# Kernel tuning notes

Measured on AMD Instinct MI355X. Metric: run time of the kernel, lower is better.

Reference implementation:

```python
import jax, jax.numpy as jnp
import numpy as np

B, N, C, H = 64, 300, 256, 8  # batch, patches (img 1x300, patch 1x1), dim, heads
STD = 0.02


def setup_inputs() -> dict:
    key = jax.random.key(0)
    ks = jax.random.split(key, 6)
    return {
        "x": jax.random.normal(ks[0], (B, N, C), jnp.float32),
        "Wqk": jax.random.normal(ks[1], (2 * C, C), jnp.float32) * STD,
        "Wv": jax.random.normal(ks[2], (C, C), jnp.float32) * STD,
        "Wpos": jax.random.normal(ks[3], (H, 3), jnp.float32) * STD,
        "bpos": jnp.zeros((H,), jnp.float32),
        "Wproj": jax.random.normal(ks[4], (C, C), jnp.float32) * STD,
        "bproj": jnp.zeros((C,), jnp.float32),
        "gating": jnp.ones((H,), jnp.float32),
    }


def _rel_indices(n):
    d = (jnp.arange(n)[None, :] - jnp.arange(n)[:, None]).astype(jnp.float32)
    return jnp.stack([d, jnp.zeros_like(d), d * d], axis=-1)  # [N, N, 3]


def reference(x, Wqk, Wv, Wpos, bpos, Wproj, bproj, gating):
    Bb, Nn, Cc = x.shape
    Hh = gating.shape[0]
    hd = Cc // Hh
    scale = hd ** -0.5

    qk = (x @ Wqk.T).reshape(Bb, Nn, 2, Hh, hd)
    q = qk[:, :, 0].transpose(0, 2, 1, 3)  # [B,H,N,hd]
    k = qk[:, :, 1].transpose(0, 2, 1, 3)

    patch_score = jax.nn.softmax(jnp.einsum('bhnd,bhmd->bhnm', q, k) * scale, axis=-1)

    rel = _rel_indices(Nn)                               # [N,N,3]
    pos_score = (rel @ Wpos.T + bpos).transpose(2, 0, 1)  # [H,N,N]
    pos_score = jax.nn.softmax(pos_score, axis=-1)

    g = jax.nn.sigmoid(gating)[None, :, None, None]       # [1,H,1,1]
    attn = (1.0 - g) * patch_score + g * pos_score[None]
    attn = attn / attn.sum(axis=-1, keepdims=True)

    v = (x @ Wv.T).reshape(Bb, Nn, Hh, hd).transpose(0, 2, 1, 3)  # [B,H,N,hd]
    out = jnp.einsum('bhnm,bhmd->bhnd', attn, v)
    out = out.transpose(0, 2, 1, 3).reshape(Bb, Nn, Cc)
    return out @ Wproj.T + bproj
```

## Files before the change

kernel.cpp:

```cpp
#include <hip/hip_runtime.h>


#define NSEQ 300
#define HEADS 8
#define HD 32

typedef short v8s __attribute__((ext_vector_type(8)));
typedef float v4f __attribute__((ext_vector_type(4)));
typedef unsigned int v4u __attribute__((ext_vector_type(4)));

__device__ __forceinline__ ushort f2bf(float f) {
    unsigned u = __float_as_uint(f);
    u = (u + 0x7FFFu + ((u >> 16) & 1u)) >> 16;
    return (ushort)u;
}

__device__ __forceinline__ unsigned pk2bf(float a, float b) {
    unsigned ua = __float_as_uint(a), ub = __float_as_uint(b);
    ua += 0x7FFFu + ((ua >> 16) & 1u);
    ub += 0x7FFFu + ((ub >> 16) & 1u);
    return __builtin_amdgcn_perm(ub, ua, 0x07060302);
}

__device__ __forceinline__ unsigned cvtpk(float a, float b) {
    unsigned r;
    asm("v_cvt_pk_bf16_f32 %0, %1, %2" : "=v"(r) : "v"(a), "v"(b));
    return r;
}

__device__ __forceinline__ float fexp2(float x) {
    float r; asm("v_exp_f32 %0, %1" : "=v"(r) : "v"(x)); return r;
}

__device__ __forceinline__ void gl_lds16(const ushort* g, ushort* l) {
    __builtin_amdgcn_global_load_lds(
        (const __attribute__((address_space(1))) void*)g,
        (__attribute__((address_space(3))) void*)l, 16, 0, 0);
}

__global__ __launch_bounds__(256) void prep_kernel(
    const float* __restrict__ Wqk, const float* __restrict__ Wv,
    const float* __restrict__ Wproj, const float* __restrict__ Wpos,
    const float* __restrict__ bpos, const float* __restrict__ gating,
    ushort* __restrict__ Wf, ushort* __restrict__ wproj_t,
    ushort* __restrict__ gpos)
{
    int bid = blockIdx.x, tid = threadIdx.x;
    if (bid < 608) {
        int sub = bid;
        int h = sub / 76;
        int i = (sub % 76) * 4 + (tid >> 6);
        int lane = tid & 63;
        ushort* gr = gpos + ((size_t)h * 304 + i) * 304;
        if (i >= NSEQ) {
#pragma unroll
            for (int t = 0; t < 5; ++t) {
                int j = lane + 64 * t;
                if (j < 304) gr[j] = 0;
            }
            return;
        }
        float w0 = Wpos[h * 3 + 0], w2 = Wpos[h * 3 + 2], bb = bpos[h];
        float g = 1.f / (1.f + __expf(-gating[h]));
        float sv[5]; float m2 = -1e30f;
#pragma unroll
        for (int t = 0; t < 5; ++t) {
            int j = lane + 64 * t;
            float d = (float)(j - i);
            float lg = fmaf(w2, d * d, fmaf(w0, d, bb));
            sv[t] = (j < NSEQ) ? lg : -1e30f;
            m2 = fmaxf(m2, sv[t]);
        }
#pragma unroll
        for (int off = 32; off > 0; off >>= 1) m2 = fmaxf(m2, __shfl_xor(m2, off));
        float sum = 0.f;
#pragma unroll
        for (int t = 0; t < 5; ++t) { sv[t] = __expf(sv[t] - m2); sum += sv[t]; }
#pragma unroll
        for (int off = 32; off > 0; off >>= 1) sum += __shfl_xor(sum, off);
        float gi = g / sum;
#pragma unroll
        for (int t = 0; t < 5; ++t) {
            int j = lane + 64 * t;
            if (j < NSEQ) gr[j] = f2bf(sv[t] * gi);
            else if (j < 304) gr[j] = 0;
        }
        return;
    }
    if (bid < 704) {
        int idx = (bid - 608) * 256 + tid;
        int c = idx & 7;
        int t = idx >> 3;
        int hk = t / 96;
        int wc = t - hk * 96;
        int h = hk >> 2, kt = hk & 3;
        const float* src;
        if (wc < 32)      src = Wqk + (size_t)(h * 32 + wc) * 256;
        else if (wc < 64) src = Wqk + (size_t)(256 + h * 32 + (wc - 32)) * 256;
        else              src = Wv + (size_t)(h * 32 + (wc - 64)) * 256;
        src += kt * 64 + c * 8;
        float4 f0 = *(const float4*)src;
        float4 f1 = *(const float4*)(src + 4);
        v4u pk = {pk2bf(f0.x, f0.y), pk2bf(f0.z, f0.w),
                  pk2bf(f1.x, f1.y), pk2bf(f1.z, f1.w)};
        *(v4u*)&Wf[((size_t)(hk * 96 + wc)) * 64 + ((c ^ (wc & 7)) * 8)] = pk;
        return;
    }
    {
        int idx = (bid - 704) * 256 + tid;
        int m = idx >> 5, ck = idx & 31;
        const float* src = Wproj + (size_t)m * 256 + ck * 8;
        int rt = m >> 7, rr = m & 127, kt = ck >> 3, c = ck & 7;
        float4 f0 = *(const float4*)src;
        float4 f1 = *(const float4*)(src + 4);
        v4u pk = {pk2bf(f0.x, f0.y), pk2bf(f0.z, f0.w),
                  pk2bf(f1.x, f1.y), pk2bf(f1.z, f1.w)};
        *(v4u*)&wproj_t[((size_t)(rt * 4 + kt) * 128 + rr) * 64 + ((c ^ (rr & 7)) * 8)] = pk;
    }
}

__global__ __launch_bounds__(256, 2) void fused_qkv_attn(
    const float* __restrict__ x, const ushort* __restrict__ Wf,
    const ushort* __restrict__ gpos, const float* __restrict__ gating,
    ushort* __restrict__ ot)
{
    __shared__ ushort smem[34816];
    ushort* Xs = smem;
    ushort* Wsh = smem + 19456;
    ushort* Qs = smem;
    ushort* Ks = smem + 12160;
    ushort* Vt = smem + 24320;

    int bid = blockIdx.x, b = bid & 63, h = bid >> 6;
    int tid = threadIdx.x, wave = tid >> 6, lane = tid & 63, li = lane & 15, qd = lane >> 4;

    const float* xb = x + (size_t)b * 300 * 256;
    const ushort* wfh = Wf + (size_t)h * 4 * 6144;

    v4f acc[5][6];
#pragma unroll
    for (int i = 0; i < 5; ++i)
#pragma unroll
        for (int j = 0; j < 6; ++j) acc[i][j] = (v4f){0.f, 0.f, 0.f, 0.f};

    for (int kt = 0; kt < 4; ++kt) {
#pragma unroll
        for (int s = 0; s < 3; ++s) {
            int c = s * 256 + tid;
            gl_lds16(wfh + (size_t)kt * 6144 + c * 8, Wsh + c * 8);
        }
#pragma unroll
        for (int it = 0; it < 19; ++it) {
            int c = it * 256 + tid;
            int r = c >> 4, q4 = c & 15;
            float4 f = {0.f, 0.f, 0.f, 0.f};
            if (r < 300) f = *(const float4*)(xb + (size_t)r * 256 + kt * 64 + q4 * 4);
            uint2 w = {cvtpk(f.x, f.y), cvtpk(f.z, f.w)};
            *(uint2*)&Xs[r * 64 + (((q4 >> 1) ^ (r & 7)) * 8) + (q4 & 1) * 4] = w;
        }
        __syncthreads();
#pragma unroll
        for (int kc = 0; kc < 64; kc += 32) {
            int cb = (kc >> 3) + qd;
            int cs = cb ^ (li & 7);
            v8s bw[6];
#pragma unroll
            for (int ct = 0; ct < 6; ++ct)
                bw[ct] = *(const v8s*)&Wsh[(ct * 16 + li) * 64 + cs * 8];
#pragma unroll
            for (int i = 0; i < 5; ++i) {
                int rt = wave + i * 4;
                if (rt < 19) {
                    v8s ax = *(const v8s*)&Xs[(rt * 16 + li) * 64 + cs * 8];
#pragma unroll
                    for (int ct = 0; ct < 6; ++ct)
                        acc[i][ct] = __builtin_amdgcn_mfma_f32_16x16x32_bf16(bw[ct], ax, acc[i][ct], 0, 0, 0);
                }
            }
        }
        __syncthreads();
    }

    const float QSC = 0.25503486063f;
#pragma unroll
    for (int i = 0; i < 5; ++i) {
        int rt = wave + i * 4;
        if (rt < 19) {
            int row = rt * 16 + li;
#pragma unroll
            for (int ct = 0; ct < 2; ++ct) {
                uint2 wq = {cvtpk(acc[i][ct][0] * QSC, acc[i][ct][1] * QSC),
                            cvtpk(acc[i][ct][2] * QSC, acc[i][ct][3] * QSC)};
                *(uint2*)&Qs[row * 40 + ct * 16 + qd * 4] = wq;
            }
#pragma unroll
            for (int ct = 2; ct < 4; ++ct) {
                uint2 wk = {cvtpk(acc[i][ct][0], acc[i][ct][1]),
                            cvtpk(acc[i][ct][2], acc[i][ct][3])};
                *(uint2*)&Ks[row * 40 + (ct - 2) * 16 + qd * 4] = wk;
            }
#pragma unroll
            for (int ct = 4; ct < 6; ++ct)
#pragma unroll
                for (int r = 0; r < 4; ++r)
                    Vt[((ct - 4) * 16 + qd * 4 + r) * 328 + row] = f2bf(acc[i][ct][r]);
        }
    }
    float g = 1.f / (1.f + __expf(-gating[h]));
    float omg = 1.f - g;
    __syncthreads();

    const ushort* ksp0 = &Ks[li * 40 + qd * 8];
    const ushort* vtp0 = &Vt[li * 328 + qd * 4];
    const ushort* vtp1 = &Vt[(16 + li) * 328 + qd * 4];
    const v4f z4 = {0.f, 0.f, 0.f, 0.f};

    for (int rg = wave; rg < 19; rg += 4) {
        int i0 = rg * 16;
        v8s bq = *(const v8s*)&Qs[(i0 + li) * 40 + qd * 8];
        const ushort* gp = gpos + ((size_t)h * 304 + (i0 + li)) * 304 + qd * 4;

        v4f Oe0 = z4, Oe1 = z4, Og0 = z4, Og1 = z4;
        float esum = 0.f;

        v8s ak0 = *(const v8s*)(ksp0);
        v8s ak1 = *(const v8s*)(ksp0 + 640);
        uint2 v0a = *(const uint2*)(vtp0);
        uint2 v0b = *(const uint2*)(vtp0 + 16);
        uint2 v1a = *(const uint2*)(vtp1);
        uint2 v1b = *(const uint2*)(vtp1 + 16);
        uint2 g0 = *(const uint2*)(gp);
        uint2 g1 = *(const uint2*)(gp + 16);
        v4f s0n = __builtin_amdgcn_mfma_f32_16x16x32_bf16(ak0, bq, z4, 0, 0, 0);
        v4f s1n = __builtin_amdgcn_mfma_f32_16x16x32_bf16(ak1, bq, z4, 0, 0, 0);

#pragma unroll 1
        for (int p = 0; p < 9; ++p) {
            v4f s0 = s0n, s1 = s1n;
            v8s b0 = __builtin_bit_cast(v8s, (v4u){v0a.x, v0a.y, v0b.x, v0b.y});
            v8s b1 = __builtin_bit_cast(v8s, (v4u){v1a.x, v1a.y, v1b.x, v1b.y});
            v8s ag = __builtin_bit_cast(v8s, (v4u){g0.x, g0.y, g1.x, g1.y});
            int nt0 = 2 * p + 2;
            int nt1 = (p < 8) ? nt0 + 1 : 18;
            ak0 = *(const v8s*)(ksp0 + nt0 * 640);
            ak1 = *(const v8s*)(ksp0 + nt1 * 640);
            v0a = *(const uint2*)(vtp0 + nt0 * 16);
            v0b = *(const uint2*)(vtp0 + nt1 * 16);
            v1a = *(const uint2*)(vtp1 + nt0 * 16);
            v1b = *(const uint2*)(vtp1 + nt1 * 16);
            g0 = *(const uint2*)(gp + nt0 * 16);
            g1 = *(const uint2*)(gp + nt1 * 16);
            s0n = __builtin_amdgcn_mfma_f32_16x16x32_bf16(ak0, bq, z4, 0, 0, 0);
            s1n = __builtin_amdgcn_mfma_f32_16x16x32_bf16(ak1, bq, z4, 0, 0, 0);

            float e0 = fexp2(s0[0]);
            float e1 = fexp2(s0[1]);
            float e2 = fexp2(s0[2]);
            float e3 = fexp2(s0[3]);
            float f0 = fexp2(s1[0]);
            float f1 = fexp2(s1[1]);
            float f2 = fexp2(s1[2]);
            float f3 = fexp2(s1[3]);
            esum += ((e0 + e1) + (e2 + e3)) + ((f0 + f1) + (f2 + f3));
            v8s ae = __builtin_bit_cast(v8s, (v4u){cvtpk(e0, e1), cvtpk(e2, e3),
                                                   cvtpk(f0, f1), cvtpk(f2, f3)});
            Oe0 = __builtin_amdgcn_mfma_f32_16x16x32_bf16(ae, b0, Oe0, 0, 0, 0);
            Oe1 = __builtin_amdgcn_mfma_f32_16x16x32_bf16(ae, b1, Oe1, 0, 0, 0);
            Og0 = __builtin_amdgcn_mfma_f32_16x16x32_bf16(ag, b0, Og0, 0, 0, 0);
            Og1 = __builtin_amdgcn_mfma_f32_16x16x32_bf16(ag, b1, Og1, 0, 0, 0);
        }
        {
            float e0 = fexp2(s0n[0]);
            float e1 = fexp2(s0n[1]);
            float e2 = fexp2(s0n[2]);
            float e3 = fexp2(s0n[3]);
            if (qd == 3) { e0 = e1 = e2 = e3 = 0.f; }
            esum += (e0 + e1) + (e2 + e3);
            v8s ae = __builtin_bit_cast(v8s, (v4u){cvtpk(e0, e1), cvtpk(e2, e3), 0u, 0u});
            v8s ag = __builtin_bit_cast(v8s, (v4u){g0.x, g0.y, 0u, 0u});
            v8s b0 = __builtin_bit_cast(v8s, (v4u){v0a.x, v0a.y, 0u, 0u});
            v8s b1 = __builtin_bit_cast(v8s, (v4u){v1a.x, v1a.y, 0u, 0u});
            Oe0 = __builtin_amdgcn_mfma_f32_16x16x32_bf16(ae, b0, Oe0, 0, 0, 0);
            Oe1 = __builtin_amdgcn_mfma_f32_16x16x32_bf16(ae, b1, Oe1, 0, 0, 0);
            Og0 = __builtin_amdgcn_mfma_f32_16x16x32_bf16(ag, b0, Og0, 0, 0, 0);
            Og1 = __builtin_amdgcn_mfma_f32_16x16x32_bf16(ag, b1, Og1, 0, 0, 0);
        }
        esum += __shfl_xor(esum, 16);
        esum += __shfl_xor(esum, 32);
        float ps = omg / esum;
        float psr[4];
#pragma unroll
        for (int r = 0; r < 4; ++r) psr[r] = __shfl(ps, qd * 4 + r);
#pragma unroll
        for (int r = 0; r < 4; ++r) {
            int row = i0 + qd * 4 + r;
            if (row < NSEQ) {
                int m = b * NSEQ + row;
                int rt = m >> 7, rr = m & 127;
                int c0 = (h & 1) * 4 + (li >> 3);
                int p2 = li & 7;
                size_t tb = ((size_t)(rt * 4 + (h >> 1)) * 128 + rr) * 64;
                ot[tb + ((c0 ^ (rr & 7)) * 8) + p2] = f2bf(fmaf(psr[r], Oe0[r], Og0[r]));
                ot[tb + (((c0 + 2) ^ (rr & 7)) * 8) + p2] = f2bf(fmaf(psr[r], Oe1[r], Og1[r]));
            }
        }
    }
}

__global__ __launch_bounds__(256, 4) void gemm_proj_mfma(
    const ushort* __restrict__ A, const ushort* __restrict__ Bw,
    const float* __restrict__ bias, float* __restrict__ out)
{
    __shared__ ushort As[64 * 64];
    __shared__ ushort Bs[128 * 64];
    int tid = threadIdx.x;
    int wave = tid >> 6, lane = tid & 63, li = lane & 15, qd = lane >> 4;
    int rh = wave >> 1, ch = wave & 1;
    int by = blockIdx.y;
    const ushort* gA = A + ((size_t)(by >> 1) * 4 * 128 + (by & 1) * 64) * 64;
    const ushort* gB = Bw + (size_t)blockIdx.x * 4 * 8192;

    v4f acc[2][4];
#pragma unroll
    for (int i = 0; i < 2; ++i)
#pragma unroll
        for (int j = 0; j < 4; ++j) acc[i][j] = (v4f){0.f, 0.f, 0.f, 0.f};

    for (int kt = 0; kt < 4; ++kt) {
#pragma unroll
        for (int s = 0; s < 2; ++s) {
            int cch = s * 256 + tid;
            gl_lds16(gA + (size_t)kt * 128 * 64 + cch * 8, As + cch * 8);
        }
#pragma unroll
        for (int s = 0; s < 4; ++s) {
            int cch = s * 256 + tid;
            gl_lds16(gB + (size_t)kt * 8192 + cch * 8, Bs + cch * 8);
        }
        __syncthreads();
#pragma unroll
        for (int kc = 0; kc < 64; kc += 32) {
            int cb = (kc >> 3) + qd;
            int cs = cb ^ (li & 7);
            v8s a[2], b[4];
#pragma unroll
            for (int mt = 0; mt < 2; ++mt)
                a[mt] = *(const v8s*)&As[(rh * 32 + mt * 16 + li) * 64 + cs * 8];
#pragma unroll
            for (int nt = 0; nt < 4; ++nt)
                b[nt] = *(const v8s*)&Bs[(ch * 64 + nt * 16 + li) * 64 + cs * 8];
#pragma unroll
            for (int mt = 0; mt < 2; ++mt)
#pragma unroll
                for (int nt = 0; nt < 4; ++nt)
                    acc[mt][nt] = __builtin_amdgcn_mfma_f32_16x16x32_bf16(b[nt], a[mt], acc[mt][nt], 0, 0, 0);
        }
        __syncthreads();
    }

#pragma unroll
    for (int mt = 0; mt < 2; ++mt) {
        int row = by * 64 + rh * 32 + mt * 16 + li;
#pragma unroll
        for (int nt = 0; nt < 4; ++nt) {
            int col = blockIdx.x * 128 + ch * 64 + nt * 16 + qd * 4;
            float4 bv = *(const float4*)&bias[col];
            float4 st = {acc[mt][nt][0] + bv.x, acc[mt][nt][1] + bv.y,
                         acc[mt][nt][2] + bv.z, acc[mt][nt][3] + bv.w};
            *(float4*)&out[(size_t)row * 256 + col] = st;
        }
    }
}

extern "C" void kernel_launch(void* const* d_in, const int* in_sizes, int n_in,
                              void* d_out, int out_size, void* d_ws, size_t ws_size,
                              hipStream_t stream) {
    const float* x      = (const float*)d_in[0];
    const float* Wqk    = (const float*)d_in[1];
    const float* Wv     = (const float*)d_in[2];
    const float* Wpos   = (const float*)d_in[3];
    const float* bpos   = (const float*)d_in[4];
    const float* Wproj  = (const float*)d_in[5];
    const float* bproj  = (const float*)d_in[6];
    const float* gating = (const float*)d_in[7];
    float* out = (float*)d_out;

    ushort* gpos     = (ushort*)d_ws;
    ushort* Wf       = gpos + 739328;
    ushort* wproj_t  = Wf + 196608;
    ushort* o_t      = wproj_t + 65536;

    prep_kernel<<<736, 256, 0, stream>>>(Wqk, Wv, Wproj, Wpos, bpos, gating,
                                         Wf, wproj_t, gpos);
    fused_qkv_attn<<<512, 256, 0, stream>>>(x, Wf, gpos, gating, o_t);
    gemm_proj_mfma<<<dim3(2, 300), 256, 0, stream>>>(o_t, wproj_t, bproj, out);
}
```

Before: 132.7 us.

## Pre-convert x to padded bf16 in prep and load via async global-to-LDS

Result: faster. 124.0 us (-6.5%).

```diff
diff --git a/kernel.cpp b/kernel.cpp
--- a/kernel.cpp
+++ b/kernel.cpp
@@ -39,15 +39,33 @@
 }
 
 __global__ __launch_bounds__(256) void prep_kernel(
+    const float* __restrict__ x,
     const float* __restrict__ Wqk, const float* __restrict__ Wv,
     const float* __restrict__ Wproj, const float* __restrict__ Wpos,
     const float* __restrict__ bpos, const float* __restrict__ gating,
-    ushort* __restrict__ Wf, ushort* __restrict__ wproj_t,
-    ushort* __restrict__ gpos)
+    ushort* __restrict__ x_bf, ushort* __restrict__ Wf,
+    ushort* __restrict__ wproj_t, ushort* __restrict__ gpos)
 {
     int bid = blockIdx.x, tid = threadIdx.x;
-    if (bid < 608) {
-        int sub = bid;
+    if (bid < 2432) {
+        int idx = bid * 256 + tid;
+        int c8 = idx & 31;
+        int mrow = idx >> 5;
+        unsigned b = (unsigned)mrow / 304u;
+        int r = mrow - (int)b * 304;
+        v4u pk = {0u, 0u, 0u, 0u};
+        if (r < 300) {
+            const float* src = x + ((size_t)b * 300 + r) * 256 + c8 * 8;
+            float4 f0 = *(const float4*)src;
+            float4 f1 = *(const float4*)(src + 4);
+            pk = (v4u){pk2bf(f0.x, f0.y), pk2bf(f0.z, f0.w),
+                       pk2bf(f1.x, f1.y), pk2bf(f1.z, f1.w)};
+        }
+        *(v4u*)&x_bf[(size_t)mrow * 256 + c8 * 8] = pk;
+        return;
+    }
+    if (bid < 3040) {
+        int sub = bid - 2432;
         int h = sub / 76;
         int i = (sub % 76) * 4 + (tid >> 6);
         int lane = tid & 63;
@@ -87,8 +105,8 @@
         }
         return;
     }
-    if (bid < 704) {
-        int idx = (bid - 608) * 256 + tid;
+    if (bid < 3136) {
+        int idx = (bid - 3040) * 256 + tid;
         int c = idx & 7;
         int t = idx >> 3;
         int hk = t / 96;
@@ -107,7 +125,7 @@
         return;
     }
     {
-        int idx = (bid - 704) * 256 + tid;
+        int idx = (bid - 3136) * 256 + tid;
         int m = idx >> 5, ck = idx & 31;
         const float* src = Wproj + (size_t)m * 256 + ck * 8;
         int rt = m >> 7, rr = m & 127, kt = ck >> 3, c = ck & 7;
@@ -120,7 +138,7 @@
 }
 
 __global__ __launch_bounds__(256, 2) void fused_qkv_attn(
-    const float* __restrict__ x, const ushort* __restrict__ Wf,
+    const ushort* __restrict__ x_bf, const ushort* __restrict__ Wf,
     const ushort* __restrict__ gpos, const float* __restrict__ gating,
     ushort* __restrict__ ot)
 {
@@ -134,7 +152,7 @@
     int bid = blockIdx.x, b = bid & 63, h = bid >> 6;
     int tid = threadIdx.x, wave = tid >> 6, lane = tid & 63, li = lane & 15, qd = lane >> 4;
 
-    const float* xb = x + (size_t)b * 300 * 256;
+    const ushort* xbb = x_bf + (size_t)b * 304 * 256;
     const ushort* wfh = Wf + (size_t)h * 4 * 6144;
 
     v4f acc[5][6];
@@ -150,13 +168,17 @@
             gl_lds16(wfh + (size_t)kt * 6144 + c * 8, Wsh + c * 8);
         }
 #pragma unroll
-        for (int it = 0; it < 19; ++it) {
-            int c = it * 256 + tid;
-            int r = c >> 4, q4 = c & 15;
-            float4 f = {0.f, 0.f, 0.f, 0.f};
-            if (r < 300) f = *(const float4*)(xb + (size_t)r * 256 + kt * 64 + q4 * 4);
-            uint2 w = {cvtpk(f.x, f.y), cvtpk(f.z, f.w)};
-            *(uint2*)&Xs[r * 64 + (((q4 >> 1) ^ (r & 7)) * 8) + (q4 & 1) * 4] = w;
+        for (int s = 0; s < 9; ++s) {
+            int cch = s * 256 + tid;
+            int r = cch >> 3, sl = cch & 7;
+            gl_lds16(xbb + (size_t)r * 256 + kt * 64 + ((sl ^ (r & 7)) * 8),
+                     Xs + cch * 8);
+        }
+        if (tid < 128) {
+            int cch = 2304 + tid;
+            int r = cch >> 3, sl = cch & 7;
+            gl_lds16(xbb + (size_t)r * 256 + kt * 64 + ((sl ^ (r & 7)) * 8),
+                     Xs + cch * 8);
         }
         __syncthreads();
 #pragma unroll
@@ -264,10 +286,12 @@
             esum += ((e0 + e1) + (e2 + e3)) + ((f0 + f1) + (f2 + f3));
             v8s ae = __builtin_bit_cast(v8s, (v4u){cvtpk(e0, e1), cvtpk(e2, e3),
                                                    cvtpk(f0, f1), cvtpk(f2, f3)});
+            __builtin_amdgcn_s_setprio(1);
             Oe0 = __builtin_amdgcn_mfma_f32_16x16x32_bf16(ae, b0, Oe0, 0, 0, 0);
             Oe1 = __builtin_amdgcn_mfma_f32_16x16x32_bf16(ae, b1, Oe1, 0, 0, 0);
             Og0 = __builtin_amdgcn_mfma_f32_16x16x32_bf16(ag, b0, Og0, 0, 0, 0);
             Og1 = __builtin_amdgcn_mfma_f32_16x16x32_bf16(ag, b1, Og1, 0, 0, 0);
+            __builtin_amdgcn_s_setprio(0);
         }
         {
             float e0 = fexp2(s0n[0]);
@@ -389,9 +413,10 @@
     ushort* Wf       = gpos + 739328;
     ushort* wproj_t  = Wf + 196608;
     ushort* o_t      = wproj_t + 65536;
-
-    prep_kernel<<<736, 256, 0, stream>>>(Wqk, Wv, Wproj, Wpos, bpos, gating,
-                                         Wf, wproj_t, gpos);
-    fused_qkv_attn<<<512, 256, 0, stream>>>(x, Wf, gpos, gating, o_t);
+    ushort* x_bf     = o_t + 4915200;
+
+    prep_kernel<<<3168, 256, 0, stream>>>(x, Wqk, Wv, Wproj, Wpos, bpos, gating,
+                                          x_bf, Wf, wproj_t, gpos);
+    fused_qkv_attn<<<512, 256, 0, stream>>>(x_bf, Wf, gpos, gating, o_t);
     gemm_proj_mfma<<<dim3(2, 300), 256, 0, stream>>>(o_t, wproj_t, bproj, out);
 }
```
